# Kernel tuning notes

Hardware: AMD Instinct MI355X
Metric: run time of the kernel (lower is better)

## Reference

```python
import jax, jax.numpy as jnp
import numpy as np

B, L, H, NH = 2, 2048, 2048, 16
K = H // NH  # q/k head dim (num_slot) = 128
EPS = 1e-5
SCALE = K ** -0.5  # fla gla default scale = key_dim**-0.5


def setup_inputs() -> dict:
    key = jax.random.key(0)
    k0, k1, k2, k3, k4 = jax.random.split(key, 5)
    std = 0.02
    return {
        "hidden_states": jax.random.normal(k0, (B, L, H), dtype=jnp.float32),
        "Wq": jax.random.normal(k1, (K, H), dtype=jnp.float32) * std,
        "Wk": jax.random.normal(k2, (K, H), dtype=jnp.float32) * std,
        "Wog": jax.random.normal(k3, (H, H), dtype=jnp.float32) * std,
        "Wig": jax.random.normal(k4, (H, H), dtype=jnp.float32) * std,
        "g_weight": jnp.ones((H,), dtype=jnp.float32),
    }


def _gla(q, k, v, g):
    # q,k: [B,L,K]; v: [B,L,V]; g: [B,L,K] (log decay per key dim)
    # recurrence: S_t = exp(g_t)[:, :, None] * S_{t-1} + k_t^T v_t ; o_t = q_t @ S_t
    def step(S, xs):
        q_t, k_t, v_t, g_t = xs  # [B,K],[B,K],[B,V],[B,K]
        S = jnp.exp(g_t)[:, :, None] * S + k_t[:, :, None] * v_t[:, None, :]
        o_t = jnp.einsum('bk,bkv->bv', q_t, S)
        return S, o_t

    S0 = jnp.zeros((q.shape[0], q.shape[2], v.shape[2]), dtype=q.dtype)
    xs = (jnp.swapaxes(q, 0, 1), jnp.swapaxes(k, 0, 1),
          jnp.swapaxes(v, 0, 1), jnp.swapaxes(g, 0, 1))
    _, o = jax.lax.scan(step, S0, xs)  # o: [L,B,V]
    return jnp.swapaxes(o, 0, 1)


def reference(hidden_states, Wq, Wk, Wog, Wig, g_weight):
    x = hidden_states
    q = x @ Wq.T  # [B,L,K]
    k_sig = jax.nn.sigmoid(x @ Wk.T)  # k = sigmoid(k_proj(x))
    q = jax.nn.silu(q) * SCALE  # swish feature map on q; fold in GLA scale
    gf = jax.nn.log_sigmoid(-k_sig)  # per-key log decay gates
    o = _gla(q, k_sig, x, gf)  # [B,L,H] (single head, V = hidden)
    # output gate + fused RMSNorm-SwishGate
    go = o @ Wog.T + x @ Wig.T
    rms = o * jax.lax.rsqrt(jnp.mean(o * o, axis=-1, keepdims=True) + EPS) * g_weight
    return rms * go * jax.nn.sigmoid(go)
```

## Files before the change

### kernel.cpp

```cpp
#include <hip/hip_runtime.h>
#include <math.h>

#define B_ 2
#define L_ 2048
#define H_ 2048
#define KD_ 128
#define SCALE_ 0.08838834764831845f
#define EPS_ 1e-5f
#define K2_ 4096

typedef __bf16 bf16x8 __attribute__((ext_vector_type(8)));
typedef float f32x4 __attribute__((ext_vector_type(4)));

static __device__ __forceinline__ float sigmoidf_(float z) {
    return 1.0f / (1.0f + __expf(-z));
}

static __device__ __forceinline__ unsigned short f2bf(float f) {
    unsigned int u = __float_as_uint(f);
    unsigned int r = (u + 0x7fffu + ((u >> 16) & 1u)) >> 16;
    return (unsigned short)r;
}

static __device__ __forceinline__ float bf2f(unsigned short s) {
    return __uint_as_float(((unsigned int)s) << 16);
}

#define ASYNC_COPY16(gsrc, ldst)                                             \
    __builtin_amdgcn_global_load_lds(                                        \
        (const __attribute__((address_space(1))) unsigned int*)(gsrc),       \
        (__attribute__((address_space(3))) unsigned int*)(ldst), 16, 0, 0)

#define JOBA_BLKS 4096
#define JOBB_BLKS 256
#define JOBC_BLKS 4096

__global__ __launch_bounds__(256) void prep_all(
    const float* __restrict__ x, const float* __restrict__ Wq,
    const float* __restrict__ Wk, const float* __restrict__ Wog,
    const float* __restrict__ Wig, unsigned short* __restrict__ Abuf,
    unsigned short* __restrict__ Wqk, unsigned short* __restrict__ Bbuf,
    float* __restrict__ rrms_acc)
{
    const int blk = blockIdx.x;
    const float* src;
    unsigned short* dst;
    if (blk < JOBA_BLKS) {
        size_t i = (size_t)blk * 256 + threadIdx.x;
        size_t m = i >> 8, c8 = (i & 255) * 8;
        src = x + m * H_ + c8;
        dst = Abuf + m * K2_ + H_ + c8;
    } else if (blk < JOBA_BLKS + JOBB_BLKS) {
        size_t i = (size_t)(blk - JOBA_BLKS) * 256 + threadIdx.x;
        if (i < 4096) rrms_acc[i] = 0.f;
        const size_t half = (size_t)KD_ * H_ / 8;
        src = ((i < half) ? Wq : Wk) + ((i < half) ? i : i - half) * 8;
        dst = Wqk + i * 8;
    } else {
        size_t i = (size_t)(blk - JOBA_BLKS - JOBB_BLKS) * 256 + threadIdx.x;
        const size_t half = (size_t)H_ * H_ / 8;
        size_t j = (i < half) ? i : i - half;
        size_t n = j >> 8, c8 = (j & 255) * 8;
        src = ((i < half) ? Wog : Wig) + n * H_ + c8;
        dst = Bbuf + n * K2_ + ((i < half) ? 0 : H_) + c8;
    }
    float4 v0 = *(const float4*)src;
    float4 v1 = *(const float4*)(src + 4);
    ushort4 a, b;
    a.x = f2bf(v0.x); a.y = f2bf(v0.y); a.z = f2bf(v0.z); a.w = f2bf(v0.w);
    b.x = f2bf(v1.x); b.y = f2bf(v1.y); b.z = f2bf(v1.z); b.w = f2bf(v1.w);
    *(ushort4*)dst = a;
    *(ushort4*)(dst + 4) = b;
}

__global__ __launch_bounds__(256) void qk_proj_mfma(
    const unsigned short* __restrict__ Abuf,
    const unsigned short* __restrict__ Wqk,
    float* __restrict__ partial)
{
    __shared__ alignas(16) unsigned short As[128 * 64];
    __shared__ alignas(16) unsigned short Bs[128 * 64];
    const int tid  = threadIdx.x;
    const int wave = tid >> 6;
    const int lane = tid & 63;
    const int m0 = blockIdx.x * 128;
    const int n0 = blockIdx.y * 128;
    const int kz = blockIdx.z * 512;
    const int wm = (wave >> 1) * 64;
    const int wn = (wave & 1) * 64;

    f32x4 acc[4][4] = {};

    const int se  = lane * 8;
    const int ldsbase = (wave * 4) * 512;
    const int frow = lane & 15;
    const int fk   = (lane >> 4) * 8;
    const int gswz = (((lane & 7) ^ (lane >> 3)) << 3);
    const int rswz = ((lane & 7) << 3);

    for (int k0 = kz; k0 < kz + 512; k0 += 64) {
        #pragma unroll
        for (int it = 0; it < 4; ++it) {
            int e = ldsbase + it * 512 + se;
            int r = e >> 6;
            const unsigned short* ga =
                Abuf + (size_t)(m0 + r) * K2_ + H_ + k0 + gswz;
            ASYNC_COPY16(ga, &As[e]);
            const unsigned short* gb = Wqk + (size_t)(n0 + r) * H_ + k0 + gswz;
            ASYNC_COPY16(gb, &Bs[e]);
        }
        __syncthreads();
        #pragma unroll
        for (int ksub = 0; ksub < 2; ++ksub) {
            bf16x8 af[4], bf[4];
            #pragma unroll
            for (int i = 0; i < 4; ++i)
                af[i] = *(const bf16x8*)(As + (wm + i * 16 + frow) * 64 +
                                         ((ksub * 32 + fk) ^ rswz));
            #pragma unroll
            for (int j = 0; j < 4; ++j)
                bf[j] = *(const bf16x8*)(Bs + (wn + j * 16 + frow) * 64 +
                                         ((ksub * 32 + fk) ^ rswz));
            #pragma unroll
            for (int i = 0; i < 4; ++i)
                #pragma unroll
                for (int j = 0; j < 4; ++j)
                    acc[i][j] = __builtin_amdgcn_mfma_f32_16x16x32_bf16(
                        af[i], bf[j], acc[i][j], 0, 0, 0);
        }
        __syncthreads();
    }

    float* pz = partial + (size_t)blockIdx.z * 4096 * 256;
    #pragma unroll
    for (int i = 0; i < 4; ++i) {
        #pragma unroll
        for (int reg = 0; reg < 4; ++reg) {
            int m = m0 + wm + i * 16 + (lane >> 4) * 4 + reg;
            #pragma unroll
            for (int j = 0; j < 4; ++j) {
                int n = n0 + wn + j * 16 + (lane & 15);
                pz[(size_t)m * 256 + n] = acc[i][j][reg];
            }
        }
    }
}

__global__ __launch_bounds__(256) void scan_scale_kernel(
    const float* __restrict__ partial,
    unsigned short* __restrict__ qt_b, unsigned short* __restrict__ kA_b,
    unsigned short* __restrict__ kB_b)
{
    const int c = blockIdx.x, b = blockIdx.y;
    const int kd = blockIdx.z * 32 + (threadIdx.x & 31);
    const int rg = threadIdx.x >> 5;
    const size_t stride = (size_t)4096 * 256;
    const int row0 = b * L_ + c * 64 + rg * 8;

    float qv[8], kv[8], gp[8];
    float run = 0.f;
    #pragma unroll
    for (int j = 0; j < 8; ++j) {
        size_t off = (size_t)(row0 + j) * 256;
        float sq = partial[off + kd] + partial[stride + off + kd]
                 + partial[2 * stride + off + kd] + partial[3 * stride + off + kd];
        float sk = partial[off + 128 + kd] + partial[stride + off + 128 + kd]
                 + partial[2 * stride + off + 128 + kd]
                 + partial[3 * stride + off + 128 + kd];
        float ksv = sigmoidf_(sk);
        qv[j] = sq * sigmoidf_(sq) * SCALE_;
        kv[j] = ksv;
        run += -log1pf(__expf(ksv));
        gp[j] = run;
    }
    __shared__ float s_seg[8][32];
    s_seg[rg][threadIdx.x & 31] = run;
    __syncthreads();
    float base = 0.f, total = 0.f;
    #pragma unroll
    for (int r = 0; r < 8; ++r) {
        float v = s_seg[r][threadIdx.x & 31];
        base += (r < rg) ? v : 0.f;
        total += v;
    }
    #pragma unroll
    for (int j = 0; j < 8; ++j) {
        float s = base + gp[j];
        size_t idx = (size_t)(row0 + j) * KD_ + kd;
        qt_b[idx] = f2bf(qv[j] * __expf(s));
        kA_b[idx] = f2bf(kv[j] * __expf(-s));
        kB_b[idx] = f2bf(kv[j] * __expf(total - s));
    }
}

__global__ __launch_bounds__(256) void p_kernel(
    const unsigned short* __restrict__ qt_b,
    const unsigned short* __restrict__ kA_b,
    const unsigned short* __restrict__ kB_b,
    unsigned short* __restrict__ Pbuf)
{
    const int c = blockIdx.x, b = blockIdx.y;
    const int tid = threadIdx.x;
    const int w = tid >> 6, l = tid & 63;
    const int lr = l & 15, lq = l >> 4;
    const int q0 = c * 64;
    const size_t rowbase = (size_t)b * L_;

    bf16x8 aq[4];
    {
        const unsigned short* qrow = qt_b + (rowbase + q0 + 16 * w + lr) * KD_;
        #pragma unroll
        for (int kt = 0; kt < 4; ++kt)
            aq[kt] = *(const bf16x8*)(qrow + kt * 32 + lq * 8);
    }
    unsigned short* pout = Pbuf + (size_t)(b * 32 + c) * 64 * 128;
    #pragma unroll
    for (int jt = 0; jt < 8; ++jt) {
        f32x4 p = {};
        const int si = jt * 16 + lr;
        const bool prev = (jt < 4);
        const bool dead = (c == 0 && prev);
        if (!dead) {
            int kp = prev ? (q0 - 64 + si) : (q0 + si - 64);
            const unsigned short* kb = (prev ? kB_b : kA_b) + (rowbase + kp) * KD_;
            #pragma unroll
            for (int kt = 0; kt < 4; ++kt) {
                bf16x8 bk = *(const bf16x8*)(kb + kt * 32 + lq * 8);
                p = __builtin_amdgcn_mfma_f32_16x16x32_bf16(aq[kt], bk, p, 0, 0, 0);
            }
        }
        #pragma unroll
        for (int reg = 0; reg < 4; ++reg) {
            int ti = 16 * w + lq * 4 + reg;
            bool keep = !dead && (si <= ti + 64);
            pout[ti * 128 + si] = keep ? f2bf(p[reg]) : (unsigned short)0;
        }
    }
}

#define SV_ 130

__global__ __launch_bounds__(256) void pv_kernel(
    const unsigned short* __restrict__ Pbuf,
    unsigned short* Abuf,
    float* __restrict__ rrms_acc)
{
    const int c  = blockIdx.x;
    const int b  = blockIdx.y;
    const int vt = blockIdx.z;
    const int tid = threadIdx.x;
    const int w = tid >> 6, l = tid & 63;
    const int lr = l & 15, lq = l >> 4;
    const int q0 = c * 64, kpos0 = q0 - 64, v0c = vt * 128;
    const size_t rowbase = (size_t)b * L_;

    __shared__ alignas(16) unsigned short Vt[128 * SV_];

    {
        const int a = tid & 15;
        const int kr0 = tid >> 4;
        for (int kr = kr0; kr < 128; kr += 16) {
            int kp = kpos0 + kr;
            ushort4 u0 = {0, 0, 0, 0}, u1 = {0, 0, 0, 0};
            if (kp >= 0) {
                const unsigned short* src =
                    Abuf + (rowbase + kp) * K2_ + H_ + v0c + a * 8;
                u0 = *(const ushort4*)src;
                u1 = *(const ushort4*)(src + 4);
            }
            unsigned short vals[8] = {u0.x, u0.y, u0.z, u0.w,
                                      u1.x, u1.y, u1.z, u1.w};
            #pragma unroll
            for (int j = 0; j < 8; ++j)
                Vt[(a * 8 + j) * SV_ + kr] = vals[j];
        }
    }

    bf16x8 ap[4];
    {
        const unsigned short* prow =
            Pbuf + ((size_t)(b * 32 + c) * 64 + 16 * w + lr) * 128;
        #pragma unroll
        for (int kt = 0; kt < 4; ++kt)
            ap[kt] = *(const bf16x8*)(prow + kt * 32 + lq * 8);
    }
    __syncthreads();

    float rsum[4] = {0.f, 0.f, 0.f, 0.f};
    #pragma unroll
    for (int jt = 0; jt < 8; ++jt) {
        f32x4 oa = {};
        const int n = jt * 16 + lr;
        #pragma unroll
        for (int kt = 0; kt < 4; ++kt) {
            const unsigned int* vp =
                (const unsigned int*)(Vt + n * SV_ + kt * 32 + lq * 8);
            union { unsigned int u[4]; bf16x8 v; } bb;
            bb.u[0] = vp[0]; bb.u[1] = vp[1]; bb.u[2] = vp[2]; bb.u[3] = vp[3];
            oa = __builtin_amdgcn_mfma_f32_16x16x32_bf16(ap[kt], bb.v, oa, 0, 0, 0);
        }
        #pragma unroll
        for (int reg = 0; reg < 4; ++reg) {
            int qrow = 16 * w + lq * 4 + reg;
            size_t orow = rowbase + q0 + qrow;
            float val = oa[reg];
            Abuf[orow * K2_ + v0c + n] = f2bf(val);
            rsum[reg] += val * val;
        }
    }
    #pragma unroll
    for (int mk = 1; mk < 16; mk <<= 1) {
        #pragma unroll
        for (int reg = 0; reg < 4; ++reg)
            rsum[reg] += __shfl_xor(rsum[reg], mk, 64);
    }
    if (lr == 0) {
        #pragma unroll
        for (int reg = 0; reg < 4; ++reg)
            atomicAdd(&rrms_acc[rowbase + q0 + 16 * w + lq * 4 + reg], rsum[reg]);
    }
}

__global__ __launch_bounds__(256) void out_gemm_mfma(
    const unsigned short* __restrict__ Abuf,
    const unsigned short* __restrict__ Bbuf,
    const float* __restrict__ gw, const float* __restrict__ rrms_acc,
    float* __restrict__ out)
{
    __shared__ alignas(16) unsigned short As[128 * 64];
    __shared__ alignas(16) unsigned short Bs[128 * 64];
    const int tid  = threadIdx.x;
    const int wave = tid >> 6;
    const int lane = tid & 63;
    const int m0 = blockIdx.x * 128;
    const int n0 = blockIdx.y * 128;
    const int wm = (wave >> 1) * 64;
    const int wn = (wave & 1) * 64;

    f32x4 acc[4][4] = {};

    const int se  = lane * 8;
    const int ldsbase = (wave * 4) * 512;
    const int frow = lane & 15;
    const int fk   = (lane >> 4) * 8;
    const int gswz = (((lane & 7) ^ (lane >> 3)) << 3);
    const int rswz = ((lane & 7) << 3);

    for (int k0 = 0; k0 < K2_; k0 += 64) {
        #pragma unroll
        for (int it = 0; it < 4; ++it) {
            int e = ldsbase + it * 512 + se;
            int r = e >> 6;
            const unsigned short* ga = Abuf + (size_t)(m0 + r) * K2_ + k0 + gswz;
            ASYNC_COPY16(ga, &As[e]);
            const unsigned short* gb = Bbuf + (size_t)(n0 + r) * K2_ + k0 + gswz;
            ASYNC_COPY16(gb, &Bs[e]);
        }
        __syncthreads();
        #pragma unroll
        for (int ksub = 0; ksub < 2; ++ksub) {
            bf16x8 af[4], bf[4];
            #pragma unroll
            for (int i = 0; i < 4; ++i)
                af[i] = *(const bf16x8*)(As + (wm + i * 16 + frow) * 64 +
                                         ((ksub * 32 + fk) ^ rswz));
            #pragma unroll
            for (int j = 0; j < 4; ++j)
                bf[j] = *(const bf16x8*)(Bs + (wn + j * 16 + frow) * 64 +
                                         ((ksub * 32 + fk) ^ rswz));
            #pragma unroll
            for (int i = 0; i < 4; ++i)
                #pragma unroll
                for (int j = 0; j < 4; ++j)
                    acc[i][j] = __builtin_amdgcn_mfma_f32_16x16x32_bf16(
                        af[i], bf[j], acc[i][j], 0, 0, 0);
        }
        __syncthreads();
    }

    #pragma unroll
    for (int i = 0; i < 4; ++i) {
        #pragma unroll
        for (int reg = 0; reg < 4; ++reg) {
            int m = m0 + wm + i * 16 + (lane >> 4) * 4 + reg;
            float rv = rsqrtf(rrms_acc[m] * (1.0f / H_) + EPS_);
            #pragma unroll
            for (int j = 0; j < 4; ++j) {
                int n = n0 + wn + j * 16 + (lane & 15);
                float go = acc[i][j][reg];
                float ov = bf2f(Abuf[(size_t)m * K2_ + n]);
                out[(size_t)m * H_ + n] = ov * rv * gw[n] * go * sigmoidf_(go);
            }
        }
    }
}

extern "C" void kernel_launch(void* const* d_in, const int* in_sizes, int n_in,
                              void* d_out, int out_size, void* d_ws, size_t ws_size,
                              hipStream_t stream) {
    (void)in_sizes; (void)n_in; (void)out_size; (void)ws_size;
    const float* x   = (const float*)d_in[0];
    const float* Wq  = (const float*)d_in[1];
    const float* Wk  = (const float*)d_in[2];
    const float* Wog = (const float*)d_in[3];
    const float* Wig = (const float*)d_in[4];
    const float* gw  = (const float*)d_in[5];
    float* out = (float*)d_out;

    const size_t MK = (size_t)B_ * L_ * KD_;
    unsigned short* Abuf = (unsigned short*)d_ws;
    unsigned short* Bbuf = Abuf + (size_t)4096 * K2_;
    unsigned short* qt_b = Bbuf + (size_t)2048 * K2_;
    unsigned short* kA_b = qt_b + MK;
    unsigned short* kB_b = kA_b + MK;
    unsigned short* Wqk  = kB_b + MK;
    unsigned short* Pbuf = Wqk + (size_t)256 * H_;
    float* partial  = (float*)(Pbuf + (size_t)64 * 64 * 128);
    float* rrms_acc = partial + (size_t)4 * 4096 * 256;

    prep_all<<<JOBA_BLKS + JOBB_BLKS + JOBC_BLKS, 256, 0, stream>>>(
        x, Wq, Wk, Wog, Wig, Abuf, Wqk, Bbuf, rrms_acc);
    qk_proj_mfma<<<dim3(32, 2, 4), 256, 0, stream>>>(Abuf, Wqk, partial);
    scan_scale_kernel<<<dim3(32, B_, 4), 256, 0, stream>>>(partial, qt_b, kA_b, kB_b);
    p_kernel<<<dim3(32, B_), 256, 0, stream>>>(qt_b, kA_b, kB_b, Pbuf);
    pv_kernel<<<dim3(32, B_, 16), 256, 0, stream>>>(Pbuf, Abuf, rrms_acc);
    out_gemm_mfma<<<dim3(32, 16), 256, 0, stream>>>(Abuf, Bbuf, gw, rrms_acc, out);
}
```

Measured before the change: 247.4 us.

## Rewrite output GEMM with 256x128 tiles, triple-buffered async loads and interleaved MFMA phases

The final output GEMM moves from a 128x128 tile with 4 waves and a single LDS buffer to a 256x128 tile with 8 waves and three LDS stages. Global-to-LDS async copies are prefetched two k-steps ahead using explicit vmcnt waits, and the LDS fragment loads are interleaved with four MFMA sub-phases under raised wave priority, so memory traffic overlaps with compute. The larger tile improves operand reuse but halves the grid to 256 blocks and uses about 144KB of LDS, which limits occupancy. The many barriers per k-step add synchronisation overhead.

New measurement: 265.0 us. 1.07x slower.

```diff
diff --git a/kernel.cpp b/kernel.cpp
--- a/kernel.cpp
+++ b/kernel.cpp
@@ -30,6 +30,13 @@
     __builtin_amdgcn_global_load_lds(                                        \
         (const __attribute__((address_space(1))) unsigned int*)(gsrc),       \
         (__attribute__((address_space(3))) unsigned int*)(ldst), 16, 0, 0)
+
+#define BAR()                                                                \
+    do {                                                                     \
+        asm volatile("" ::: "memory");                                       \
+        __builtin_amdgcn_s_barrier();                                        \
+        asm volatile("" ::: "memory");                                       \
+    } while (0)
 
 #define JOBA_BLKS 4096
 #define JOBB_BLKS 256
@@ -321,72 +328,160 @@
     }
 }
 
-__global__ __launch_bounds__(256) void out_gemm_mfma(
+__global__ __launch_bounds__(512, 2) void out_gemm_mfma(
     const unsigned short* __restrict__ Abuf,
     const unsigned short* __restrict__ Bbuf,
     const float* __restrict__ gw, const float* __restrict__ rrms_acc,
     float* __restrict__ out)
 {
-    __shared__ alignas(16) unsigned short As[128 * 64];
-    __shared__ alignas(16) unsigned short Bs[128 * 64];
+    __shared__ alignas(16) unsigned short As[3 * 256 * 64];
+    __shared__ alignas(16) unsigned short Bs[3 * 128 * 64];
     const int tid  = threadIdx.x;
-    const int wave = tid >> 6;
+    const int w    = tid >> 6;
     const int lane = tid & 63;
-    const int m0 = blockIdx.x * 128;
+    const int wr   = w >> 1;
+    const int wc   = w & 1;
+    const int m0 = blockIdx.x * 256;
     const int n0 = blockIdx.y * 128;
-    const int wm = (wave >> 1) * 64;
-    const int wn = (wave & 1) * 64;
+
+    const int frow = lane & 15;
+    const int fkb  = (lane >> 4) << 3;
+    const int rxor = (lane & 7) << 3;
+
+    const int srow = tid >> 3;
+    const int scol = (((tid & 7) ^ (srow & 7)) << 3);
+    const unsigned short* agsrc = Abuf + (size_t)(m0 + srow) * K2_ + scol;
+    const unsigned short* bgsrc = Bbuf + (size_t)(n0 + srow) * K2_ + scol;
+    unsigned short* As_dst = As + tid * 8;
+    unsigned short* Bs_dst = Bs + tid * 8;
+
+#define STAGE_A_(cb, k0)                                                     \
+    {                                                                        \
+        _Pragma("unroll")                                                    \
+        for (int it_ = 0; it_ < 4; ++it_)                                    \
+            ASYNC_COPY16(agsrc + (size_t)(it_ * 64) * K2_ + (k0),            \
+                         As_dst + (cb) * 16384 + it_ * 4096);                \
+    }
+#define STAGE_B_(cb, k0)                                                     \
+    {                                                                        \
+        _Pragma("unroll")                                                    \
+        for (int it_ = 0; it_ < 2; ++it_)                                    \
+            ASYNC_COPY16(bgsrc + (size_t)(it_ * 64) * K2_ + (k0),            \
+                         Bs_dst + (cb) * 8192 + it_ * 4096);                 \
+    }
+#define LDA_(buf, i_, ks_)                                                   \
+    (*(const bf16x8*)((buf) + (wr * 64 + (i_) * 16 + frow) * 64 +            \
+                      (((ks_) * 32 + fkb) ^ rxor)))
+#define LDB_(buf, j_, ks_)                                                   \
+    (*(const bf16x8*)((buf) + (wc * 64 + (j_) * 16 + frow) * 64 +            \
+                      (((ks_) * 32 + fkb) ^ rxor)))
+#define MFMA_(a_, b_, c_)                                                    \
+    (c_) = __builtin_amdgcn_mfma_f32_16x16x32_bf16((a_), (b_), (c_), 0, 0, 0)
 
     f32x4 acc[4][4] = {};
 
-    const int se  = lane * 8;
-    const int ldsbase = (wave * 4) * 512;
-    const int frow = lane & 15;
-    const int fk   = (lane >> 4) * 8;
-    const int gswz = (((lane & 7) ^ (lane >> 3)) << 3);
-    const int rswz = ((lane & 7) << 3);
-
-    for (int k0 = 0; k0 < K2_; k0 += 64) {
-        #pragma unroll
-        for (int it = 0; it < 4; ++it) {
-            int e = ldsbase + it * 512 + se;
-            int r = e >> 6;
-            const unsigned short* ga = Abuf + (size_t)(m0 + r) * K2_ + k0 + gswz;
-            ASYNC_COPY16(ga, &As[e]);
-            const unsigned short* gb = Bbuf + (size_t)(n0 + r) * K2_ + k0 + gswz;
-            ASYNC_COPY16(gb, &Bs[e]);
-        }
-        __syncthreads();
-        #pragma unroll
-        for (int ksub = 0; ksub < 2; ++ksub) {
-            bf16x8 af[4], bf[4];
-            #pragma unroll
-            for (int i = 0; i < 4; ++i)
-                af[i] = *(const bf16x8*)(As + (wm + i * 16 + frow) * 64 +
-                                         ((ksub * 32 + fk) ^ rswz));
-            #pragma unroll
-            for (int j = 0; j < 4; ++j)
-                bf[j] = *(const bf16x8*)(Bs + (wn + j * 16 + frow) * 64 +
-                                         ((ksub * 32 + fk) ^ rswz));
-            #pragma unroll
-            for (int i = 0; i < 4; ++i)
-                #pragma unroll
-                for (int j = 0; j < 4; ++j)
-                    acc[i][j] = __builtin_amdgcn_mfma_f32_16x16x32_bf16(
-                        af[i], bf[j], acc[i][j], 0, 0, 0);
-        }
-        __syncthreads();
-    }
+    STAGE_A_(0, 0); STAGE_B_(0, 0);
+    STAGE_A_(1, 64); STAGE_B_(1, 64);
+    asm volatile("s_waitcnt vmcnt(6)" ::: "memory");
+    BAR();
+
+    int cur = 0;
+    for (int t = 0; t < 64; ++t) {
+        const unsigned short* Ab = As + cur * 16384;
+        const unsigned short* Bb = Bs + cur * 8192;
+        int stg = cur + 2; if (stg >= 3) stg -= 3;
+        const int kpre = (t + 2) * 64;
+        const bool pre = (t + 2 < 64);
+        bf16x8 af[2][2], bfr[4][2];
+
+        #pragma unroll
+        for (int ii = 0; ii < 2; ++ii) {
+            af[ii][0] = LDA_(Ab, ii, 0);
+            af[ii][1] = LDA_(Ab, ii, 1);
+        }
+        #pragma unroll
+        for (int j = 0; j < 2; ++j) {
+            bfr[j][0] = LDB_(Bb, j, 0);
+            bfr[j][1] = LDB_(Bb, j, 1);
+        }
+        if (pre) STAGE_A_(stg, kpre);
+        BAR();
+        __builtin_amdgcn_s_setprio(1);
+        #pragma unroll
+        for (int ii = 0; ii < 2; ++ii)
+            #pragma unroll
+            for (int j = 0; j < 2; ++j) {
+                MFMA_(af[ii][0], bfr[j][0], acc[ii][j]);
+                MFMA_(af[ii][1], bfr[j][1], acc[ii][j]);
+            }
+        __builtin_amdgcn_s_setprio(0);
+        BAR();
+
+        #pragma unroll
+        for (int j = 0; j < 2; ++j) {
+            bfr[2 + j][0] = LDB_(Bb, 2 + j, 0);
+            bfr[2 + j][1] = LDB_(Bb, 2 + j, 1);
+        }
+        if (pre) STAGE_B_(stg, kpre);
+        BAR();
+        __builtin_amdgcn_s_setprio(1);
+        #pragma unroll
+        for (int ii = 0; ii < 2; ++ii)
+            #pragma unroll
+            for (int j = 0; j < 2; ++j) {
+                MFMA_(af[ii][0], bfr[2 + j][0], acc[ii][2 + j]);
+                MFMA_(af[ii][1], bfr[2 + j][1], acc[ii][2 + j]);
+            }
+        __builtin_amdgcn_s_setprio(0);
+        BAR();
+
+        #pragma unroll
+        for (int ii = 0; ii < 2; ++ii) {
+            af[ii][0] = LDA_(Ab, 2 + ii, 0);
+            af[ii][1] = LDA_(Ab, 2 + ii, 1);
+        }
+        BAR();
+        __builtin_amdgcn_s_setprio(1);
+        #pragma unroll
+        for (int ii = 0; ii < 2; ++ii)
+            #pragma unroll
+            for (int j = 0; j < 2; ++j) {
+                MFMA_(af[ii][0], bfr[j][0], acc[2 + ii][j]);
+                MFMA_(af[ii][1], bfr[j][1], acc[2 + ii][j]);
+            }
+        __builtin_amdgcn_s_setprio(0);
+        BAR();
+
+        __builtin_amdgcn_s_setprio(1);
+        #pragma unroll
+        for (int ii = 0; ii < 2; ++ii)
+            #pragma unroll
+            for (int j = 0; j < 2; ++j) {
+                MFMA_(af[ii][0], bfr[2 + j][0], acc[2 + ii][2 + j]);
+                MFMA_(af[ii][1], bfr[2 + j][1], acc[2 + ii][2 + j]);
+            }
+        __builtin_amdgcn_s_setprio(0);
+        if (pre) { asm volatile("s_waitcnt vmcnt(6)" ::: "memory"); }
+        else     { asm volatile("s_waitcnt vmcnt(0)" ::: "memory"); }
+        BAR();
+        cur = cur + 1; if (cur == 3) cur = 0;
+    }
+
+#undef STAGE_A_
+#undef STAGE_B_
+#undef LDA_
+#undef LDB_
+#undef MFMA_
 
     #pragma unroll
     for (int i = 0; i < 4; ++i) {
         #pragma unroll
         for (int reg = 0; reg < 4; ++reg) {
-            int m = m0 + wm + i * 16 + (lane >> 4) * 4 + reg;
+            int m = m0 + wr * 64 + i * 16 + (lane >> 4) * 4 + reg;
             float rv = rsqrtf(rrms_acc[m] * (1.0f / H_) + EPS_);
             #pragma unroll
             for (int j = 0; j < 4; ++j) {
-                int n = n0 + wn + j * 16 + (lane & 15);
+                int n = n0 + wc * 64 + j * 16 + (lane & 15);
                 float go = acc[i][j][reg];
                 float ov = bf2f(Abuf[(size_t)m * K2_ + n]);
                 out[(size_t)m * H_ + n] = ov * rv * gw[n] * go * sigmoidf_(go);
@@ -424,5 +519,5 @@
     scan_scale_kernel<<<dim3(32, B_, 4), 256, 0, stream>>>(partial, qt_b, kA_b, kB_b);
     p_kernel<<<dim3(32, B_), 256, 0, stream>>>(qt_b, kA_b, kB_b, Pbuf);
     pv_kernel<<<dim3(32, B_, 16), 256, 0, stream>>>(Pbuf, Abuf, rrms_acc);
-    out_gemm_mfma<<<dim3(32, 16), 256, 0, stream>>>(Abuf, Bbuf, gw, rrms_acc, out);
-}
+    out_gemm_mfma<<<dim3(16, 16), 512, 0, stream>>>(Abuf, Bbuf, gw, rrms_acc, out);
+}
```
